# Optimization experiments

Measured on AMD Instinct MI355X. Metric: run time of the kernel, lower is better.

The kernel has to match this reference:

```python
import jax, jax.numpy as jnp
import numpy as np

EPS = 1e-6
THRESHOLD = 0.5


def ternarize(weight):
    # absmax scale along last dim (in_features)
    scale = jnp.clip(jnp.max(jnp.abs(weight), axis=-1, keepdims=True), EPS, None)
    normalized = weight / scale
    ternary = jnp.where(normalized > THRESHOLD, 1.0,
                        jnp.where(normalized < -THRESHOLD, -1.0, 0.0)).astype(weight.dtype)
    return ternary * scale


def setup_inputs() -> dict:
    key = jax.random.key(0)
    k1, k2, k3 = jax.random.split(key, 3)
    B, S, D_in, D_out = 4, 4096, 2048, 2048
    x = jax.random.normal(k1, (B, S, D_in), dtype=jnp.float32)
    # kaiming-uniform-ish init
    bound_w = (6.0 / D_in) ** 0.5 / (1.0 + 5.0) ** 0.5
    weight = jax.random.uniform(k2, (D_out, D_in), dtype=jnp.float32, minval=-bound_w, maxval=bound_w)
    bound_b = 1.0 / D_in ** 0.5
    bias = jax.random.uniform(k3, (D_out,), dtype=jnp.float32, minval=-bound_b, maxval=bound_b)
    return {"x": x, "weight": weight, "bias": bias}


def reference(x, weight, bias):
    qw = ternarize(weight)  # [out, in]
    # F.linear: x @ qw.T + bias
    return jnp.einsum('bsi,oi->bso', x, qw) + bias
```

## Files before the change

kernel.cpp:

```cpp
#include <hip/hip_runtime.h>
#include <hip/hip_bf16.h>
#include <stdint.h>


#define M_DIM 16384
#define N_DIM 2048
#define K_DIM 2048

#define BM 128
#define BN 128
#define BK 32

typedef __bf16 bf16x8 __attribute__((ext_vector_type(8)));
typedef float f32x4 __attribute__((ext_vector_type(4)));

__global__ __launch_bounds__(256) void cvt_x_k(
    const float* __restrict__ x, __hip_bfloat16* __restrict__ xb) {
  const size_t i = ((size_t)blockIdx.x * 256 + threadIdx.x) * 8;
  const float4 a = *(const float4*)(x + i);
  const float4 b = *(const float4*)(x + i + 4);
  bf16x8 o;
  o[0] = (__bf16)a.x; o[1] = (__bf16)a.y; o[2] = (__bf16)a.z; o[3] = (__bf16)a.w;
  o[4] = (__bf16)b.x; o[5] = (__bf16)b.y; o[6] = (__bf16)b.z; o[7] = (__bf16)b.w;
  *(bf16x8*)((__bf16*)xb + i) = o;
}

__global__ __launch_bounds__(256) void ternarize_k(
    const float* __restrict__ w,
    __hip_bfloat16* __restrict__ qw,
    float* __restrict__ scales) {
  const int row = blockIdx.x;
  const float* wr = w + (size_t)row * K_DIM;

  float m = 0.0f;
  for (int k = threadIdx.x; k < K_DIM; k += 256)
    m = fmaxf(m, fabsf(wr[k]));

  for (int off = 32; off > 0; off >>= 1)
    m = fmaxf(m, __shfl_down(m, off, 64));
  __shared__ float wmax[4];
  if ((threadIdx.x & 63) == 0) wmax[threadIdx.x >> 6] = m;
  __syncthreads();
  float scale = fmaxf(fmaxf(wmax[0], wmax[1]), fmaxf(wmax[2], wmax[3]));
  scale = fmaxf(scale, 1e-6f);
  if (threadIdx.x == 0) scales[row] = scale;

  for (int k = threadIdx.x; k < K_DIM; k += 256) {
    const float v = wr[k] / scale;
    const float t = (v > 0.5f) ? 1.0f : ((v < -0.5f) ? -1.0f : 0.0f);
    qw[(size_t)row * K_DIM + k] = __float2bfloat16(t);
  }
}

static __device__ __forceinline__ void async_cp16(const __hip_bfloat16* g,
                                                  __hip_bfloat16* l) {
  __builtin_amdgcn_global_load_lds(
      (__attribute__((address_space(1))) void*)const_cast<__hip_bfloat16*>(g),
      (__attribute__((address_space(3))) void*)(l), 16, 0, 0);
}

__global__ __launch_bounds__(256) void gemm_bt_k(
    const __hip_bfloat16* __restrict__ A,
    const __hip_bfloat16* __restrict__ B,
    const float* __restrict__ scales,
    const float* __restrict__ bias,
    float* __restrict__ C) {
  __shared__ __hip_bfloat16 As[BM * BK];
  __shared__ __hip_bfloat16 Bs[BN * BK];

  const int tid = threadIdx.x;
  const int wave = tid >> 6;
  const int lane = tid & 63;
  const int quad = lane >> 4;
  const int lrow = lane & 15;
  const int wm = wave >> 1;
  const int wn = wave & 1;

  const int m0 = blockIdx.y * BM;
  const int n0 = blockIdx.x * BN;

  const int c = tid;
  const __hip_bfloat16* Ag0 = A + (size_t)(m0 + (c >> 2)) * K_DIM + (c & 3) * 8;
  const __hip_bfloat16* Ag1 = A + (size_t)(m0 + ((c + 256) >> 2)) * K_DIM + (c & 3) * 8;
  const __hip_bfloat16* Bg0 = B + (size_t)(n0 + (c >> 2)) * K_DIM + (c & 3) * 8;
  const __hip_bfloat16* Bg1 = B + (size_t)(n0 + ((c + 256) >> 2)) * K_DIM + (c & 3) * 8;

  __hip_bfloat16* As_w0 = As + wave * 512;
  __hip_bfloat16* As_w1 = As + wave * 512 + 2048;
  __hip_bfloat16* Bs_w0 = Bs + wave * 512;
  __hip_bfloat16* Bs_w1 = Bs + wave * 512 + 2048;

  f32x4 acc[4][4] = {};

  for (int kk = 0; kk < K_DIM; kk += BK) {
    __syncthreads();
    async_cp16(Ag0 + kk, As_w0);
    async_cp16(Ag1 + kk, As_w1);
    async_cp16(Bg0 + kk, Bs_w0);
    async_cp16(Bg1 + kk, Bs_w1);
    __syncthreads();

    bf16x8 af[4], bfr[4];
    #pragma unroll
    for (int i = 0; i < 4; ++i)
      af[i] = *(const bf16x8*)(As + (wm * 64 + i * 16 + lrow) * BK + quad * 8);
    #pragma unroll
    for (int i = 0; i < 4; ++i)
      bfr[i] = *(const bf16x8*)(Bs + (wn * 64 + i * 16 + lrow) * BK + quad * 8);

    #pragma unroll
    for (int i = 0; i < 4; ++i)
      #pragma unroll
      for (int j = 0; j < 4; ++j)
        acc[i][j] = __builtin_amdgcn_mfma_f32_16x16x32_bf16(af[i], bfr[j], acc[i][j], 0, 0, 0);
  }

  #pragma unroll
  for (int j = 0; j < 4; ++j) {
    const int col = n0 + wn * 64 + j * 16 + lrow;
    const float s = scales[col];
    const float b = bias[col];
    #pragma unroll
    for (int i = 0; i < 4; ++i) {
      const int rbase = m0 + wm * 64 + i * 16 + quad * 4;
      #pragma unroll
      for (int r = 0; r < 4; ++r)
        C[(size_t)(rbase + r) * N_DIM + col] = acc[i][j][r] * s + b;
    }
  }
}

extern "C" void kernel_launch(void* const* d_in, const int* in_sizes, int n_in,
                              void* d_out, int out_size, void* d_ws, size_t ws_size,
                              hipStream_t stream) {
  const float* x    = (const float*)d_in[0];
  const float* w    = (const float*)d_in[1];
  const float* bias = (const float*)d_in[2];
  float* out = (float*)d_out;

  __hip_bfloat16* xb = (__hip_bfloat16*)d_ws;
  __hip_bfloat16* qw = (__hip_bfloat16*)((char*)d_ws + (size_t)M_DIM * K_DIM * 2);
  float* scales = (float*)((char*)d_ws + (size_t)M_DIM * K_DIM * 2 + (size_t)N_DIM * K_DIM * 2);

  cvt_x_k<<<dim3((M_DIM * (size_t)K_DIM) / (256 * 8)), dim3(256), 0, stream>>>(x, xb);
  ternarize_k<<<dim3(N_DIM), dim3(256), 0, stream>>>(w, qw, scales);
  gemm_bt_k<<<dim3(N_DIM / BN, M_DIM / BM), dim3(256), 0, stream>>>(xb, qw, scales, bias, out);
}
```

Measured before the change: 396.4 us.

## Rewrite GEMM with 256x256 tiles, double-buffered LDS prefetch, swizzle and wave priority

The bf16 GEMM moves to 256x256x64 tiles with 512 threads and 8 waves. It double-buffers LDS using async global-to-LDS loads issued two k-steps ahead, XOR-swizzles the LDS layout to avoid bank conflicts, and remaps block IDs for better cache locality. MFMA phases are interleaved with LDS reads and prefetches, using s_setprio and explicit vmcnt waits. The goal is to hide memory latency and raise data reuse per tile. In exchange it uses 128KB of LDS and many accumulator registers, which limits occupancy, and it adds complex barrier logic.

```diff
diff --git a/kernel.cpp b/kernel.cpp
--- a/kernel.cpp
+++ b/kernel.cpp
@@ -7,9 +7,10 @@
 #define N_DIM 2048
 #define K_DIM 2048
 
-#define BM 128
-#define BN 128
-#define BK 32
+#define BM 256
+#define BN 256
+#define BK 64
+#define NT (K_DIM / BK)
 
 typedef __bf16 bf16x8 __attribute__((ext_vector_type(8)));
 typedef float f32x4 __attribute__((ext_vector_type(4)));
@@ -52,82 +53,177 @@
   }
 }
 
-static __device__ __forceinline__ void async_cp16(const __hip_bfloat16* g,
-                                                  __hip_bfloat16* l) {
+static __device__ __forceinline__ void gload16(const __hip_bfloat16* g,
+                                               char* l) {
   __builtin_amdgcn_global_load_lds(
       (__attribute__((address_space(1))) void*)const_cast<__hip_bfloat16*>(g),
       (__attribute__((address_space(3))) void*)(l), 16, 0, 0);
 }
 
-__global__ __launch_bounds__(256) void gemm_bt_k(
+#define MFMA_(d, a, b) \
+  d = __builtin_amdgcn_mfma_f32_16x16x32_bf16(a, b, d, 0, 0, 0)
+
+__global__ __launch_bounds__(512, 2) void gemm_bt_k(
     const __hip_bfloat16* __restrict__ A,
     const __hip_bfloat16* __restrict__ B,
     const float* __restrict__ scales,
     const float* __restrict__ bias,
     float* __restrict__ C) {
-  __shared__ __hip_bfloat16 As[BM * BK];
-  __shared__ __hip_bfloat16 Bs[BN * BK];
-
-  const int tid = threadIdx.x;
+  __shared__ __align__(128) char lds[131072];
+
+  const int tid  = threadIdx.x;
   const int wave = tid >> 6;
   const int lane = tid & 63;
   const int quad = lane >> 4;
   const int lrow = lane & 15;
-  const int wm = wave >> 1;
-  const int wn = wave & 1;
-
-  const int m0 = blockIdx.y * BM;
-  const int n0 = blockIdx.x * BN;
-
-  const int c = tid;
-  const __hip_bfloat16* Ag0 = A + (size_t)(m0 + (c >> 2)) * K_DIM + (c & 3) * 8;
-  const __hip_bfloat16* Ag1 = A + (size_t)(m0 + ((c + 256) >> 2)) * K_DIM + (c & 3) * 8;
-  const __hip_bfloat16* Bg0 = B + (size_t)(n0 + (c >> 2)) * K_DIM + (c & 3) * 8;
-  const __hip_bfloat16* Bg1 = B + (size_t)(n0 + ((c + 256) >> 2)) * K_DIM + (c & 3) * 8;
-
-  __hip_bfloat16* As_w0 = As + wave * 512;
-  __hip_bfloat16* As_w1 = As + wave * 512 + 2048;
-  __hip_bfloat16* Bs_w0 = Bs + wave * 512;
-  __hip_bfloat16* Bs_w1 = Bs + wave * 512 + 2048;
-
-  f32x4 acc[4][4] = {};
-
-  for (int kk = 0; kk < K_DIM; kk += BK) {
-    __syncthreads();
-    async_cp16(Ag0 + kk, As_w0);
-    async_cp16(Ag1 + kk, As_w1);
-    async_cp16(Bg0 + kk, Bs_w0);
-    async_cp16(Bg1 + kk, Bs_w1);
-    __syncthreads();
-
-    bf16x8 af[4], bfr[4];
-    #pragma unroll
-    for (int i = 0; i < 4; ++i)
-      af[i] = *(const bf16x8*)(As + (wm * 64 + i * 16 + lrow) * BK + quad * 8);
-    #pragma unroll
-    for (int i = 0; i < 4; ++i)
-      bfr[i] = *(const bf16x8*)(Bs + (wn * 64 + i * 16 + lrow) * BK + quad * 8);
-
-    #pragma unroll
-    for (int i = 0; i < 4; ++i)
-      #pragma unroll
-      for (int j = 0; j < 4; ++j)
-        acc[i][j] = __builtin_amdgcn_mfma_f32_16x16x32_bf16(af[i], bfr[j], acc[i][j], 0, 0, 0);
+  const int wr = wave >> 2;
+  const int wc = wave & 3;
+
+  const int orig = blockIdx.x;
+  const int wg = (orig & 7) * 64 + (orig >> 3);
+  const int bx = wg & 7;
+  const int by = wg >> 3;
+  const int m0 = by * BM;
+  const int n0 = bx * BN;
+
+  const int srow  = tid >> 3;
+  const int scol8 = (tid & 7) ^ (srow & 7);
+  const __hip_bfloat16* Ag = A + (size_t)(m0 + srow) * K_DIM + scol8 * 8;
+  const __hip_bfloat16* Bg = B + (size_t)(n0 + srow) * K_DIM + scol8 * 8;
+  const int ldsw = wave * 1024;
+
+  const int axor  = lrow & 7;
+  const int aOff0 = lrow * 128 + ((0 + quad) ^ axor) * 16;
+  const int aOff1 = lrow * 128 + ((4 + quad) ^ axor) * 16;
+  const int bRow  = (wc & 1) * 64 + lrow;
+  const int bOff0 = bRow * 128 + ((0 + quad) ^ axor) * 16;
+  const int bOff1 = bRow * 128 + ((4 + quad) ^ axor) * 16;
+  const int aHalf = wr * 16384;
+  const int bHalf = 32768 + (wc >> 1) * 16384;
+
+#define LDA(buf, m, s) \
+  (*(const bf16x8*)(lds + (buf) + aHalf + (m) * 2048 + ((s) ? aOff1 : aOff0)))
+#define LDB(buf, n, s) \
+  (*(const bf16x8*)(lds + (buf) + bHalf + (n) * 2048 + ((s) ? bOff1 : bOff0)))
+
+  auto STAGE_A = [&](int bufOff, int h, int kk) {
+    const __hip_bfloat16* g = Ag + (size_t)h * 128 * K_DIM + kk;
+    char* l = lds + bufOff + h * 16384 + ldsw;
+    gload16(g, l);
+    gload16(g + 64 * K_DIM, l + 8192);
+  };
+  auto STAGE_B = [&](int bufOff, int h, int kk) {
+    const __hip_bfloat16* g = Bg + (size_t)h * 128 * K_DIM + kk;
+    char* l = lds + bufOff + 32768 + h * 16384 + ldsw;
+    gload16(g, l);
+    gload16(g + 64 * K_DIM, l + 8192);
+  };
+
+  f32x4 acc[8][4] = {};
+
+  STAGE_A(0, 0, 0);  STAGE_A(0, 1, 0);  STAGE_B(0, 0, 0);  STAGE_B(0, 1, 0);
+  STAGE_A(65536, 0, BK); STAGE_A(65536, 1, BK);
+  STAGE_B(65536, 0, BK); STAGE_B(65536, 1, BK);
+  asm volatile("s_waitcnt vmcnt(8)" ::: "memory");
+  __builtin_amdgcn_s_barrier();
+
+  for (int t = 0; t < NT; ++t) {
+    const int bufOff = (t & 1) << 16;
+    const int kk2 = (t + 2) * BK;
+    const bool pf = (t + 2) < NT;
+
+    bf16x8 af0[4][2], af1[4][2], bf0[2][2], bf1[2][2];
+
+#pragma unroll
+    for (int m = 0; m < 4; ++m) {
+      af0[m][0] = LDA(bufOff, m, 0);
+      af0[m][1] = LDA(bufOff, m, 1);
+    }
+#pragma unroll
+    for (int n = 0; n < 2; ++n) {
+      bf0[n][0] = LDB(bufOff, n, 0);
+      bf0[n][1] = LDB(bufOff, n, 1);
+    }
+    __builtin_amdgcn_s_barrier();
+    __builtin_amdgcn_s_setprio(1);
+#pragma unroll
+    for (int m = 0; m < 4; ++m)
+#pragma unroll
+      for (int n = 0; n < 2; ++n) {
+        MFMA_(acc[m][n], af0[m][0], bf0[n][0]);
+        MFMA_(acc[m][n], af0[m][1], bf0[n][1]);
+      }
+    __builtin_amdgcn_s_setprio(0);
+    __builtin_amdgcn_s_barrier();
+
+#pragma unroll
+    for (int m = 0; m < 4; ++m) {
+      af1[m][0] = LDA(bufOff, m + 4, 0);
+      af1[m][1] = LDA(bufOff, m + 4, 1);
+    }
+    __builtin_amdgcn_s_barrier();
+    __builtin_amdgcn_s_setprio(1);
+#pragma unroll
+    for (int m = 0; m < 4; ++m)
+#pragma unroll
+      for (int n = 0; n < 2; ++n) {
+        MFMA_(acc[m + 4][n], af1[m][0], bf0[n][0]);
+        MFMA_(acc[m + 4][n], af1[m][1], bf0[n][1]);
+      }
+    __builtin_amdgcn_s_setprio(0);
+    __builtin_amdgcn_s_barrier();
+
+#pragma unroll
+    for (int n = 0; n < 2; ++n) {
+      bf1[n][0] = LDB(bufOff, n + 2, 0);
+      bf1[n][1] = LDB(bufOff, n + 2, 1);
+    }
+    if (pf) { STAGE_A(bufOff, 0, kk2); STAGE_A(bufOff, 1, kk2); }
+    __builtin_amdgcn_s_barrier();
+    __builtin_amdgcn_s_setprio(1);
+#pragma unroll
+    for (int m = 0; m < 4; ++m)
+#pragma unroll
+      for (int n = 0; n < 2; ++n) {
+        MFMA_(acc[m + 4][n + 2], af1[m][0], bf1[n][0]);
+        MFMA_(acc[m + 4][n + 2], af1[m][1], bf1[n][1]);
+      }
+    __builtin_amdgcn_s_setprio(0);
+    __builtin_amdgcn_s_barrier();
+
+    if (pf) { STAGE_B(bufOff, 0, kk2); STAGE_B(bufOff, 1, kk2); }
+    __builtin_amdgcn_s_barrier();
+    __builtin_amdgcn_s_setprio(1);
+#pragma unroll
+    for (int m = 0; m < 4; ++m)
+#pragma unroll
+      for (int n = 0; n < 2; ++n) {
+        MFMA_(acc[m][n + 2], af0[m][0], bf1[n][0]);
+        MFMA_(acc[m][n + 2], af0[m][1], bf1[n][1]);
+      }
+    __builtin_amdgcn_s_setprio(0);
+    if (t < NT - 2)
+      asm volatile("s_waitcnt vmcnt(8)" ::: "memory");
+    else
+      asm volatile("s_waitcnt vmcnt(0)" ::: "memory");
+    __builtin_amdgcn_s_barrier();
   }
 
-  #pragma unroll
-  for (int j = 0; j < 4; ++j) {
-    const int col = n0 + wn * 64 + j * 16 + lrow;
+#pragma unroll
+  for (int n = 0; n < 4; ++n) {
+    const int col = n0 + wc * 64 + n * 16 + lrow;
     const float s = scales[col];
     const float b = bias[col];
-    #pragma unroll
-    for (int i = 0; i < 4; ++i) {
-      const int rbase = m0 + wm * 64 + i * 16 + quad * 4;
-      #pragma unroll
+#pragma unroll
+    for (int m = 0; m < 8; ++m) {
+      const int rbase = m0 + wr * 128 + m * 16 + quad * 4;
+#pragma unroll
       for (int r = 0; r < 4; ++r)
-        C[(size_t)(rbase + r) * N_DIM + col] = acc[i][j][r] * s + b;
+        C[(size_t)(rbase + r) * N_DIM + col] = acc[m][n][r] * s + b;
     }
   }
+#undef LDA
+#undef LDB
 }
 
 extern "C" void kernel_launch(void* const* d_in, const int* in_sizes, int n_in,
@@ -144,5 +240,5 @@
 
   cvt_x_k<<<dim3((M_DIM * (size_t)K_DIM) / (256 * 8)), dim3(256), 0, stream>>>(x, xb);
   ternarize_k<<<dim3(N_DIM), dim3(256), 0, stream>>>(w, qw, scales);
-  gemm_bt_k<<<dim3(N_DIM / BN, M_DIM / BM), dim3(256), 0, stream>>>(xb, qw, scales, bias, out);
-}
+  gemm_bt_k<<<dim3((M_DIM / BM) * (N_DIM / BN)), dim3(512), 0, stream>>>(xb, qw, scales, bias, out);
+}
```

New measurement: 367.0 us. 7.4% less time.
